# Kernel tuning notes

Measured on AMD Instinct MI355X. Metric: run time of the kernel, lower is better.

Reference implementation:

```python
import jax, jax.numpy as jnp
import numpy as np

NEG = -1000000.0

def setup_inputs() -> dict:
    key = jax.random.key(0)
    ks = jax.random.split(key, 7)
    B, Lq, Lk, Dq, Dk, Dv, H = 4, 256, 1024, 512, 512, 512, 256
    return {
        "query": jax.random.normal(ks[0], (B, Lq, Dq), dtype=jnp.float32),
        "key": jax.random.normal(ks[1], (B, Lk, Dk), dtype=jnp.float32),
        "value": jax.random.normal(ks[2], (B, Lk, Dv), dtype=jnp.float32),
        "valid_len": jax.random.randint(ks[3], (B,), 1, Lk + 1),
        "Wq": jax.random.normal(ks[4], (Dq, H), dtype=jnp.float32) * (1.0 / np.sqrt(Dq)),
        "Wk": jax.random.normal(ks[5], (Dk, H), dtype=jnp.float32) * (1.0 / np.sqrt(Dk)),
        "wv": jax.random.normal(ks[6], (H,), dtype=jnp.float32) * (1.0 / np.sqrt(H)),
    }

def reference(query, key, value, valid_len, Wq, Wk, wv):
    # projections: [B,Lq,H], [B,Lk,H]
    q = jnp.einsum("bqd,dh->bqh", query, Wq)
    k = jnp.einsum("bkd,dh->bkh", key, Wk)
    # broadcast-add + tanh: [B,Lq,Lk,H]
    features = jnp.tanh(q[:, :, None, :] + k[:, None, :, :])
    # score projection to scalar: [B,Lq,Lk]
    score = jnp.einsum("bqkh,h->bqk", features, wv)
    # masked softmax over keys (valid_len per batch, broadcast over queries)
    Lk = key.shape[1]
    mask = jnp.arange(Lk)[None, None, :] < valid_len[:, None, None]
    score = jnp.where(mask, score, NEG)
    attn = jax.nn.softmax(score, axis=-1)
    # weighted sum of values: [B,Lq,Dv]  (dropout is identity in eval)
    return jnp.einsum("bqk,bkv->bqv", attn, value)
```

## Files before the change

kernel.cpp:

```cpp
#include <hip/hip_runtime.h>

typedef __attribute__((ext_vector_type(8))) short short8v;
typedef __attribute__((ext_vector_type(4))) float float4v;
typedef unsigned int uint;

#define TWO_LOG2E 2.8853900817779268f
#define LOG2E     1.4426950408889634f

__device__ inline uint rne_bf16(float x) {
    uint u = __float_as_uint(x);
    return (u + 0x7fffu + ((u >> 16) & 1u)) >> 16;
}
__device__ inline uint pack_hi_lo(float a0, float a1, uint& lo_pack) {
    const uint h0 = rne_bf16(a0), h1 = rne_bf16(a1);
    const float f0 = __uint_as_float(h0 << 16), f1 = __uint_as_float(h1 << 16);
    const float l0 = a0 - f0, l1 = a1 - f1;
    lo_pack = (rne_bf16(l1) << 16) | rne_bf16(l0);
    return (h1 << 16) | h0;
}

__global__ __launch_bounds__(256) void prep_a(
    const float* __restrict__ query, const float* __restrict__ key,
    const int* __restrict__ vlen,
    ushort* __restrict__ A_hi, ushort* __restrict__ A_lo)
{
    const int t = blockIdx.x * 256 + threadIdx.x;
    const int row = t >> 6;
    const int cg = (t & 63) * 8;
    if (row >= 1024) {
        const int kr = (row - 1024) & 1023, b = (row - 1024) >> 10;
        if ((kr & ~63) >= vlen[b]) return;
    }
    const float* src = (row < 1024) ? (query + (size_t)row * 512 + cg)
                                    : (key + (size_t)(row - 1024) * 512 + cg);
    const float4 x0 = *(const float4*)src;
    const float4 x1 = *(const float4*)(src + 4);
    uint h0, h1, h2, h3, l0, l1, l2, l3;
    h0 = pack_hi_lo(x0.x, x0.y, l0);
    h1 = pack_hi_lo(x0.z, x0.w, l1);
    h2 = pack_hi_lo(x1.x, x1.y, l2);
    h3 = pack_hi_lo(x1.z, x1.w, l3);
    *(uint4*)(A_hi + (size_t)row * 512 + cg) = make_uint4(h0, h1, h2, h3);
    *(uint4*)(A_lo + (size_t)row * 512 + cg) = make_uint4(l0, l1, l2, l3);
}

__global__ __launch_bounds__(256) void prep_w(
    const float* __restrict__ Wq, const float* __restrict__ Wk,
    ushort* __restrict__ WT_hi, ushort* __restrict__ WT_lo)
{
    const int t = blockIdx.x * 256 + threadIdx.x;
    const int n = t & 255;
    const int kg = ((t >> 8) & 63) * 8;
    const int w = t >> 14;
    const float* W = w ? Wk : Wq;
    float x[8];
    #pragma unroll
    for (int i = 0; i < 8; ++i) x[i] = W[(size_t)(kg + i) * 256 + n];
    uint h0, h1, h2, h3, l0, l1, l2, l3;
    h0 = pack_hi_lo(x[0], x[1], l0);
    h1 = pack_hi_lo(x[2], x[3], l1);
    h2 = pack_hi_lo(x[4], x[5], l2);
    h3 = pack_hi_lo(x[6], x[7], l3);
    const size_t off = ((size_t)w * 256 + n) * 512 + kg;
    *(uint4*)(WT_hi + off) = make_uint4(h0, h1, h2, h3);
    *(uint4*)(WT_lo + off) = make_uint4(l0, l1, l2, l3);
}

__global__ __launch_bounds__(256) void prep_v(
    const float* __restrict__ value, const int* __restrict__ vlen,
    ushort* __restrict__ VT_hi, ushort* __restrict__ VT_lo)
{
    __shared__ float t[64][69];
    const int b = blockIdx.z;
    const int k0 = blockIdx.y * 64, n0 = blockIdx.x * 64;
    const int kendB = (vlen[b] + 31) & ~31;
    if (k0 >= kendB) return;

    const int tid = threadIdx.x;
    const int n_in = (tid & 15) * 4, k_in = tid >> 4;
    const float* src = value + ((size_t)b * 1024 + k0 + k_in) * 512 + n0 + n_in;
    #pragma unroll
    for (int p = 0; p < 4; ++p) {
        const float4 x = *(const float4*)(src + (size_t)p * 16 * 512);
        t[k_in + p * 16][n_in + 0] = x.x;
        t[k_in + p * 16][n_in + 1] = x.y;
        t[k_in + p * 16][n_in + 2] = x.z;
        t[k_in + p * 16][n_in + 3] = x.w;
    }
    __syncthreads();

    const int rn = tid >> 2, c0 = (tid & 3) * 16;
    uint hp[8], lp[8];
    #pragma unroll
    for (int i = 0; i < 8; ++i)
        hp[i] = pack_hi_lo(t[c0 + 2 * i][rn], t[c0 + 2 * i + 1][rn], lp[i]);
    const size_t off = ((size_t)b * 512 + n0 + rn) * 1024 + k0 + c0;
    *(uint4*)(VT_hi + off) = make_uint4(hp[0], hp[1], hp[2], hp[3]);
    *(uint4*)(VT_hi + off + 8) = make_uint4(hp[4], hp[5], hp[6], hp[7]);
    *(uint4*)(VT_lo + off) = make_uint4(lp[0], lp[1], lp[2], lp[3]);
    *(uint4*)(VT_lo + off + 8) = make_uint4(lp[4], lp[5], lp[6], lp[7]);
}

#define LOADF(s, kbase) { const int ko = (kbase) + half * 8;                \
    _Pragma("unroll") for (int f = 0; f < 2; ++f) {                         \
        ah##s[f] = *(const short8v*)(a_h + (size_t)(f * 16) * 512 + ko);    \
        al##s[f] = *(const short8v*)(a_l + (size_t)(f * 16) * 512 + ko); }  \
    _Pragma("unroll") for (int f = 0; f < 4; ++f) {                         \
        bh##s[f] = *(const short8v*)(wt_h + (size_t)(f * 16) * 512 + ko);   \
        bl##s[f] = *(const short8v*)(wt_l + (size_t)(f * 16) * 512 + ko); } }

#define MFMAS(s)                                                                          \
    _Pragma("unroll") for (int mf = 0; mf < 2; ++mf)                                      \
    _Pragma("unroll") for (int nf = 0; nf < 4; ++nf) {                                    \
        acc[mf][nf] = __builtin_amdgcn_mfma_f32_16x16x32_bf16(ah##s[mf], bh##s[nf], acc[mf][nf], 0, 0, 0); \
        acc[mf][nf] = __builtin_amdgcn_mfma_f32_16x16x32_bf16(ah##s[mf], bl##s[nf], acc[mf][nf], 0, 0, 0); \
        acc[mf][nf] = __builtin_amdgcn_mfma_f32_16x16x32_bf16(al##s[mf], bh##s[nf], acc[mf][nf], 0, 0, 0); }

__global__ __launch_bounds__(64) void proj_mfma(
    const ushort* __restrict__ A_hi, const ushort* __restrict__ A_lo,
    const ushort* __restrict__ WT_hi, const ushort* __restrict__ WT_lo,
    const int* __restrict__ valid_len,
    float* __restrict__ EqT, float* __restrict__ EkT)
{
    const int lane = threadIdx.x;
    const int n0 = blockIdx.x * 64;
    const int m0 = blockIdx.y * 32;
    const bool isq = (m0 < 1024);
    int b = 0, kk0 = 0;
    if (!isq) {
        kk0 = (m0 - 1024) & 1023;
        b = (m0 - 1024) >> 10;
        if (kk0 >= valid_len[b]) return;
    }
    const int r = lane & 15, half = lane >> 4;
    const size_t wsel = isq ? 0 : (size_t)256 * 512;
    const ushort* wt_h = WT_hi + wsel + (size_t)(n0 + r) * 512;
    const ushort* wt_l = WT_lo + wsel + (size_t)(n0 + r) * 512;
    const ushort* a_h = A_hi + (size_t)(m0 + r) * 512;
    const ushort* a_l = A_lo + (size_t)(m0 + r) * 512;

    float4v acc[2][4] = {{{0.f}}};
    short8v ah0[2], al0[2], bh0[4], bl0[4];
    short8v ah1[2], al1[2], bh1[4], bl1[4];

    LOADF(0, 0);
    for (int kt = 0; kt < 512; kt += 64) {
        LOADF(1, kt + 32);
        MFMAS(0);
        if (kt + 64 < 512) LOADF(0, kt + 64);
        MFMAS(1);
    }

    #pragma unroll
    for (int mf = 0; mf < 2; ++mf) {
        #pragma unroll
        for (int nf = 0; nf < 4; ++nf) {
            float4v e;
            #pragma unroll
            for (int i = 0; i < 4; ++i)
                e[i] = __builtin_amdgcn_exp2f(acc[mf][nf][i] * TWO_LOG2E);
            if (isq) {
                *(float4v*)(EqT + (size_t)(n0 + nf * 16 + r) * 1024 +
                            m0 + mf * 16 + half * 4) = e;
            } else {
                *(float4v*)(EkT + (size_t)(b * 256 + n0 + nf * 16 + r) * 1024 +
                            kk0 + mf * 16 + half * 4) = e;
            }
        }
    }
}

__global__ __launch_bounds__(512) void score_softmax_kernel(
    const float* __restrict__ EqT, const float* __restrict__ EkT,
    const float* __restrict__ wv, const int* __restrict__ valid_len,
    ushort* __restrict__ attn_hi, ushort* __restrict__ attn_lo)
{
    __shared__ float wv_s[256];
    __shared__ float eq4_s[256 * 4];
    __shared__ float red[8][4];

    const int tid = threadIdx.x;
    const int b = blockIdx.x >> 6;
    const int q0 = (blockIdx.x & 63) << 2;

    const int vlen = valid_len[b];
    const int k0 = tid * 2;
    const bool v0 = (k0 < vlen), v1 = (k0 + 1 < vlen);

    if (tid < 256) {
        wv_s[tid] = wv[tid];
        *(float4*)&eq4_s[tid * 4] =
            *(const float4*)(EqT + (size_t)tid * 1024 + b * 256 + q0);
    }
    __syncthreads();

    float acc[4][2] = {};

    if (v0) {
        const float* ekp = EkT + (size_t)(b * 256) * 1024 + k0;
        #pragma unroll 4
        for (int h = 0; h < 256; ++h) {
            const float2 ek = *(const float2*)(ekp + (size_t)h * 1024);
            const float4 eq = *(const float4*)&eq4_s[h * 4];
            const float w = wv_s[h];
            acc[0][0] = fmaf(w, __builtin_amdgcn_rcpf(fmaf(eq.x, ek.x, 1.f)), acc[0][0]);
            acc[0][1] = fmaf(w, __builtin_amdgcn_rcpf(fmaf(eq.x, ek.y, 1.f)), acc[0][1]);
            acc[1][0] = fmaf(w, __builtin_amdgcn_rcpf(fmaf(eq.y, ek.x, 1.f)), acc[1][0]);
            acc[1][1] = fmaf(w, __builtin_amdgcn_rcpf(fmaf(eq.y, ek.y, 1.f)), acc[1][1]);
            acc[2][0] = fmaf(w, __builtin_amdgcn_rcpf(fmaf(eq.z, ek.x, 1.f)), acc[2][0]);
            acc[2][1] = fmaf(w, __builtin_amdgcn_rcpf(fmaf(eq.z, ek.y, 1.f)), acc[2][1]);
            acc[3][0] = fmaf(w, __builtin_amdgcn_rcpf(fmaf(eq.w, ek.x, 1.f)), acc[3][0]);
            acc[3][1] = fmaf(w, __builtin_amdgcn_rcpf(fmaf(eq.w, ek.y, 1.f)), acc[3][1]);
        }
    }

    float s[4][2], m[4];
    #pragma unroll
    for (int q = 0; q < 4; ++q) {
        s[q][0] = -2.f * acc[q][0];
        s[q][1] = -2.f * acc[q][1];
        float mm = -1e30f;
        if (v0) mm = s[q][0];
        if (v1) mm = fmaxf(mm, s[q][1]);
        m[q] = mm;
    }
    #pragma unroll
    for (int o = 32; o; o >>= 1) {
        #pragma unroll
        for (int q = 0; q < 4; ++q) m[q] = fmaxf(m[q], __shfl_xor(m[q], o));
    }
    const int wid = tid >> 6;
    if ((tid & 63) == 0) {
        #pragma unroll
        for (int q = 0; q < 4; ++q) red[wid][q] = m[q];
    }
    __syncthreads();
    #pragma unroll
    for (int q = 0; q < 4; ++q) {
        float mm = red[0][q];
        #pragma unroll
        for (int w = 1; w < 8; ++w) mm = fmaxf(mm, red[w][q]);
        m[q] = mm;
    }
    __syncthreads();

    float p[4][2], l[4];
    #pragma unroll
    for (int q = 0; q < 4; ++q) {
        p[q][0] = v0 ? __builtin_amdgcn_exp2f((s[q][0] - m[q]) * LOG2E) : 0.f;
        p[q][1] = v1 ? __builtin_amdgcn_exp2f((s[q][1] - m[q]) * LOG2E) : 0.f;
        l[q] = p[q][0] + p[q][1];
    }
    #pragma unroll
    for (int o = 32; o; o >>= 1) {
        #pragma unroll
        for (int q = 0; q < 4; ++q) l[q] += __shfl_xor(l[q], o);
    }
    if ((tid & 63) == 0) {
        #pragma unroll
        for (int q = 0; q < 4; ++q) red[wid][q] = l[q];
    }
    __syncthreads();
    #pragma unroll
    for (int q = 0; q < 4; ++q) {
        float ss = red[0][q];
        #pragma unroll
        for (int w = 1; w < 8; ++w) ss += red[w][q];
        const float rl = __builtin_amdgcn_rcpf(ss);
        const float a0 = p[q][0] * rl, a1 = p[q][1] * rl;
        uint lo;
        const uint hi = pack_hi_lo(a0, a1, lo);
        const size_t off = (size_t)(b * 256 + q0 + q) * 1024 + k0;
        *(uint*)(attn_hi + off) = hi;
        *(uint*)(attn_lo + off) = lo;
    }
}

#define PVLOAD(s, ko) {                                   \
    ah##s = *(const short8v*)(ah_p + (ko));               \
    al##s = *(const short8v*)(al_p + (ko));               \
    bh0##s = *(const short8v*)(bh_p + (ko));              \
    bl0##s = *(const short8v*)(bl_p + (ko));              \
    bh1##s = *(const short8v*)(bh_p + 16 * 1024 + (ko));  \
    bl1##s = *(const short8v*)(bl_p + 16 * 1024 + (ko)); }

#define PVMFMA(s) {                                                              \
    acc0 = __builtin_amdgcn_mfma_f32_16x16x32_bf16(ah##s, bh0##s, acc0, 0, 0, 0); \
    acc0 = __builtin_amdgcn_mfma_f32_16x16x32_bf16(ah##s, bl0##s, acc0, 0, 0, 0); \
    acc0 = __builtin_amdgcn_mfma_f32_16x16x32_bf16(al##s, bh0##s, acc0, 0, 0, 0); \
    acc1 = __builtin_amdgcn_mfma_f32_16x16x32_bf16(ah##s, bh1##s, acc1, 0, 0, 0); \
    acc1 = __builtin_amdgcn_mfma_f32_16x16x32_bf16(ah##s, bl1##s, acc1, 0, 0, 0); \
    acc1 = __builtin_amdgcn_mfma_f32_16x16x32_bf16(al##s, bh1##s, acc1, 0, 0, 0); }

__global__ __launch_bounds__(64) void pv_mfma(
    const ushort* __restrict__ attn_hi, const ushort* __restrict__ attn_lo,
    const ushort* __restrict__ VT_hi, const ushort* __restrict__ VT_lo,
    const int* __restrict__ valid_len,
    float* __restrict__ out)
{
    const int lane = threadIdx.x;
    const int n0 = blockIdx.x * 32;
    const int q0 = blockIdx.y * 16;
    const int b = blockIdx.z;
    const int r = lane & 15, half = lane >> 4;
    const int kend = (valid_len[b] + 31) & ~31;

    const ushort* ah_p = attn_hi + (size_t)(b * 256 + q0 + r) * 1024 + half * 8;
    const ushort* al_p = attn_lo + (size_t)(b * 256 + q0 + r) * 1024 + half * 8;
    const ushort* bh_p = VT_hi + (size_t)(b * 512 + n0 + r) * 1024 + half * 8;
    const ushort* bl_p = VT_lo + (size_t)(b * 512 + n0 + r) * 1024 + half * 8;

    float4v acc0 = {0.f}, acc1 = {0.f};
    short8v ah0, al0, bh00, bl00, bh10, bl10;
    short8v ah1, al1, bh01, bl01, bh11, bl11;

    PVLOAD(0, 0);
    for (int kt = 0; kt < kend; kt += 64) {
        if (kt + 32 < kend) PVLOAD(1, kt + 32);
        PVMFMA(0);
        if (kt + 64 < kend) PVLOAD(0, kt + 64);
        if (kt + 32 < kend) PVMFMA(1);
    }

    float* op = out + (size_t)b * 256 * 512 + (size_t)(q0 + half * 4) * 512 + n0 + r;
    #pragma unroll
    for (int i = 0; i < 4; ++i) {
        op[(size_t)i * 512] = acc0[i];
        op[(size_t)i * 512 + 16] = acc1[i];
    }
}

extern "C" void kernel_launch(void* const* d_in, const int* in_sizes, int n_in,
                              void* d_out, int out_size, void* d_ws, size_t ws_size,
                              hipStream_t stream)
{
    const float* query = (const float*)d_in[0];
    const float* key   = (const float*)d_in[1];
    const float* value = (const float*)d_in[2];
    const int*   vlen  = (const int*)d_in[3];
    const float* Wq    = (const float*)d_in[4];
    const float* Wk    = (const float*)d_in[5];
    const float* wv    = (const float*)d_in[6];
    float* out = (float*)d_out;

    float*  EqT     = (float*)d_ws;
    float*  EkT     = EqT + 262144;
    ushort* A_hi    = (ushort*)(EkT + 1048576);
    ushort* A_lo    = A_hi + 2621440;
    ushort* WT_hi   = A_lo + 2621440;
    ushort* WT_lo   = WT_hi + 262144;
    ushort* attn_hi = WT_lo + 262144;
    ushort* attn_lo = attn_hi + 1048576;
    ushort* VT_hi   = attn_lo + 1048576;
    ushort* VT_lo   = VT_hi + 2097152;

    hipLaunchKernelGGL(prep_w, dim3(128), dim3(256), 0, stream,
                       Wq, Wk, WT_hi, WT_lo);
    hipLaunchKernelGGL(prep_a, dim3(1280), dim3(256), 0, stream,
                       query, key, vlen, A_hi, A_lo);
    hipLaunchKernelGGL(prep_v, dim3(8, 16, 4), dim3(256), 0, stream,
                       value, vlen, VT_hi, VT_lo);
    hipLaunchKernelGGL(proj_mfma, dim3(4, 160), dim3(64), 0, stream,
                       A_hi, A_lo, WT_hi, WT_lo, vlen, EqT, EkT);
    hipLaunchKernelGGL(score_softmax_kernel, dim3(256), dim3(512), 0, stream,
                       EqT, EkT, wv, vlen, attn_hi, attn_lo);
    hipLaunchKernelGGL(pv_mfma, dim3(16, 16, 4), dim3(64), 0, stream,
                       attn_hi, attn_lo, VT_hi, VT_lo, vlen, out);
}
```

Baseline: 87.03 us.

## Split score/softmax into H-partitioned partial-score kernel plus separate softmax

The fused score+softmax kernel launched only 256 blocks, one per 4 queries. The new code computes scores in a separate kernel with 2048 blocks. Each block covers one quarter of the hidden dim, a 256-key tile and 8 queries, and skips key tiles entirely past valid_len. A second softmax kernel sums the four partial-score planes, applies the masked softmax and writes the hi/lo bf16 attention split. The aim is more occupancy and parallelism for the rcp-bound scoring loop, at the cost of a 16 MB partial buffer written and re-read through memory plus an extra launch.

Result: no change. 87.76 us (+0.8%).

```diff
diff --git a/kernel.cpp b/kernel.cpp
--- a/kernel.cpp
+++ b/kernel.cpp
@@ -170,59 +170,84 @@
     }
 }
 
-__global__ __launch_bounds__(512) void score_softmax_kernel(
+__global__ __launch_bounds__(256) void score_partial(
     const float* __restrict__ EqT, const float* __restrict__ EkT,
     const float* __restrict__ wv, const int* __restrict__ valid_len,
+    float* __restrict__ P)
+{
+    __shared__ float eqs[64][8];
+    __shared__ float wvs[64];
+
+    const int idx = blockIdx.x;
+    const int hq = idx & 3;
+    const int kt = (idx >> 2) & 3;
+    const int qg = (idx >> 4) & 31;
+    const int b  = idx >> 9;
+
+    const int vlen = valid_len[b];
+    if (kt * 256 >= vlen) return;
+
+    const int tid = threadIdx.x;
+    const int k = kt * 256 + tid;
+    const int q0 = qg * 8;
+    const int h0 = hq * 64;
+
+    if (tid < 64) wvs[tid] = wv[h0 + tid];
+    #pragma unroll
+    for (int r = 0; r < 2; ++r) {
+        const int i = r * 256 + tid;
+        const int h = i >> 3, q = i & 7;
+        eqs[h][q] = EqT[(size_t)(h0 + h) * 1024 + b * 256 + q0 + q];
+    }
+    __syncthreads();
+
+    float acc[8] = {};
+    if (k < vlen) {
+        const float* ekp = EkT + (size_t)(b * 256 + h0) * 1024 + k;
+        #pragma unroll 2
+        for (int h = 0; h < 64; ++h) {
+            const float ek = ekp[(size_t)h * 1024];
+            const float w = wvs[h];
+            const float4 e0 = *(const float4*)&eqs[h][0];
+            const float4 e1 = *(const float4*)&eqs[h][4];
+            acc[0] = fmaf(w, __builtin_amdgcn_rcpf(fmaf(e0.x, ek, 1.f)), acc[0]);
+            acc[1] = fmaf(w, __builtin_amdgcn_rcpf(fmaf(e0.y, ek, 1.f)), acc[1]);
+            acc[2] = fmaf(w, __builtin_amdgcn_rcpf(fmaf(e0.z, ek, 1.f)), acc[2]);
+            acc[3] = fmaf(w, __builtin_amdgcn_rcpf(fmaf(e0.w, ek, 1.f)), acc[3]);
+            acc[4] = fmaf(w, __builtin_amdgcn_rcpf(fmaf(e1.x, ek, 1.f)), acc[4]);
+            acc[5] = fmaf(w, __builtin_amdgcn_rcpf(fmaf(e1.y, ek, 1.f)), acc[5]);
+            acc[6] = fmaf(w, __builtin_amdgcn_rcpf(fmaf(e1.z, ek, 1.f)), acc[6]);
+            acc[7] = fmaf(w, __builtin_amdgcn_rcpf(fmaf(e1.w, ek, 1.f)), acc[7]);
+        }
+    }
+
+    float* Pq = P + (size_t)hq * 1048576;
+    #pragma unroll
+    for (int qi = 0; qi < 8; ++qi)
+        Pq[(size_t)(b * 256 + q0 + qi) * 1024 + k] = acc[qi];
+}
+
+__global__ __launch_bounds__(1024) void softmax_kernel(
+    const float* __restrict__ P, const int* __restrict__ valid_len,
     ushort* __restrict__ attn_hi, ushort* __restrict__ attn_lo)
 {
-    __shared__ float wv_s[256];
-    __shared__ float eq4_s[256 * 4];
-    __shared__ float red[8][4];
+    __shared__ float red[16][4];
 
     const int tid = threadIdx.x;
     const int b = blockIdx.x >> 6;
     const int q0 = (blockIdx.x & 63) << 2;
 
     const int vlen = valid_len[b];
-    const int k0 = tid * 2;
-    const bool v0 = (k0 < vlen), v1 = (k0 + 1 < vlen);
-
-    if (tid < 256) {
-        wv_s[tid] = wv[tid];
-        *(float4*)&eq4_s[tid * 4] =
-            *(const float4*)(EqT + (size_t)tid * 1024 + b * 256 + q0);
-    }
-    __syncthreads();
-
-    float acc[4][2] = {};
-
-    if (v0) {
-        const float* ekp = EkT + (size_t)(b * 256) * 1024 + k0;
-        #pragma unroll 4
-        for (int h = 0; h < 256; ++h) {
-            const float2 ek = *(const float2*)(ekp + (size_t)h * 1024);
-            const float4 eq = *(const float4*)&eq4_s[h * 4];
-            const float w = wv_s[h];
-            acc[0][0] = fmaf(w, __builtin_amdgcn_rcpf(fmaf(eq.x, ek.x, 1.f)), acc[0][0]);
-            acc[0][1] = fmaf(w, __builtin_amdgcn_rcpf(fmaf(eq.x, ek.y, 1.f)), acc[0][1]);
-            acc[1][0] = fmaf(w, __builtin_amdgcn_rcpf(fmaf(eq.y, ek.x, 1.f)), acc[1][0]);
-            acc[1][1] = fmaf(w, __builtin_amdgcn_rcpf(fmaf(eq.y, ek.y, 1.f)), acc[1][1]);
-            acc[2][0] = fmaf(w, __builtin_amdgcn_rcpf(fmaf(eq.z, ek.x, 1.f)), acc[2][0]);
-            acc[2][1] = fmaf(w, __builtin_amdgcn_rcpf(fmaf(eq.z, ek.y, 1.f)), acc[2][1]);
-            acc[3][0] = fmaf(w, __builtin_amdgcn_rcpf(fmaf(eq.w, ek.x, 1.f)), acc[3][0]);
-            acc[3][1] = fmaf(w, __builtin_amdgcn_rcpf(fmaf(eq.w, ek.y, 1.f)), acc[3][1]);
-        }
-    }
-
-    float s[4][2], m[4];
+    const int k = tid;
+    const bool v = (k < vlen);
+
+    float s[4], m[4];
     #pragma unroll
     for (int q = 0; q < 4; ++q) {
-        s[q][0] = -2.f * acc[q][0];
-        s[q][1] = -2.f * acc[q][1];
-        float mm = -1e30f;
-        if (v0) mm = s[q][0];
-        if (v1) mm = fmaxf(mm, s[q][1]);
-        m[q] = mm;
+        const size_t off = (size_t)(b * 256 + q0 + q) * 1024 + k;
+        s[q] = -2.f * (P[off] + P[off + 1048576] +
+                       P[off + 2097152] + P[off + 3145728]);
+        m[q] = v ? s[q] : -1e30f;
     }
     #pragma unroll
     for (int o = 32; o; o >>= 1) {
@@ -239,17 +264,16 @@
     for (int q = 0; q < 4; ++q) {
         float mm = red[0][q];
         #pragma unroll
-        for (int w = 1; w < 8; ++w) mm = fmaxf(mm, red[w][q]);
+        for (int w = 1; w < 16; ++w) mm = fmaxf(mm, red[w][q]);
         m[q] = mm;
     }
     __syncthreads();
 
-    float p[4][2], l[4];
+    float p[4], l[4];
     #pragma unroll
     for (int q = 0; q < 4; ++q) {
-        p[q][0] = v0 ? __builtin_amdgcn_exp2f((s[q][0] - m[q]) * LOG2E) : 0.f;
-        p[q][1] = v1 ? __builtin_amdgcn_exp2f((s[q][1] - m[q]) * LOG2E) : 0.f;
-        l[q] = p[q][0] + p[q][1];
+        p[q] = v ? __builtin_amdgcn_exp2f((s[q] - m[q]) * LOG2E) : 0.f;
+        l[q] = p[q];
     }
     #pragma unroll
     for (int o = 32; o; o >>= 1) {
@@ -265,14 +289,13 @@
     for (int q = 0; q < 4; ++q) {
         float ss = red[0][q];
         #pragma unroll
-        for (int w = 1; w < 8; ++w) ss += red[w][q];
-        const float rl = __builtin_amdgcn_rcpf(ss);
-        const float a0 = p[q][0] * rl, a1 = p[q][1] * rl;
-        uint lo;
-        const uint hi = pack_hi_lo(a0, a1, lo);
-        const size_t off = (size_t)(b * 256 + q0 + q) * 1024 + k0;
-        *(uint*)(attn_hi + off) = hi;
-        *(uint*)(attn_lo + off) = lo;
+        for (int w = 1; w < 16; ++w) ss += red[w][q];
+        const float a = p[q] * __builtin_amdgcn_rcpf(ss);
+        const uint hi = rne_bf16(a);
+        const float lo = a - __uint_as_float(hi << 16);
+        const size_t off = (size_t)(b * 256 + q0 + q) * 1024 + k;
+        attn_hi[off] = (ushort)hi;
+        attn_lo[off] = (ushort)rne_bf16(lo);
     }
 }
 
@@ -345,7 +368,8 @@
 
     float*  EqT     = (float*)d_ws;
     float*  EkT     = EqT + 262144;
-    ushort* A_hi    = (ushort*)(EkT + 1048576);
+    float*  P       = EkT + 1048576;
+    ushort* A_hi    = (ushort*)(P + 4194304);
     ushort* A_lo    = A_hi + 2621440;
     ushort* WT_hi   = A_lo + 2621440;
     ushort* WT_lo   = WT_hi + 262144;
@@ -362,8 +386,10 @@
                        value, vlen, VT_hi, VT_lo);
     hipLaunchKernelGGL(proj_mfma, dim3(4, 160), dim3(64), 0, stream,
                        A_hi, A_lo, WT_hi, WT_lo, vlen, EqT, EkT);
-    hipLaunchKernelGGL(score_softmax_kernel, dim3(256), dim3(512), 0, stream,
-                       EqT, EkT, wv, vlen, attn_hi, attn_lo);
+    hipLaunchKernelGGL(score_partial, dim3(2048), dim3(256), 0, stream,
+                       EqT, EkT, wv, vlen, P);
+    hipLaunchKernelGGL(softmax_kernel, dim3(256), dim3(1024), 0, stream,
+                       P, vlen, attn_hi, attn_lo);
     hipLaunchKernelGGL(pv_mfma, dim3(16, 16, 4), dim3(64), 0, stream,
                        attn_hi, attn_lo, VT_hi, VT_lo, vlen, out);
 }
```
